# Kernel tuning notes

Hardware: AMD Instinct MI355X
Metric: run time of the kernel (lower is better)

The kernel has to match this reference:

```python
import jax, jax.numpy as jnp
import numpy as np

B, T, C = 16, 1024, 128  # batch, block_size (window length), n_hembd


def setup_inputs() -> dict:
    key = jax.random.key(0)
    k1, k2, k3 = jax.random.split(key, 3)
    Q = jax.random.normal(k1, (B, T, C), dtype=jnp.float32)
    K = jax.random.normal(k2, (B, 2 * T - 1, C), dtype=jnp.float32)
    # learned parameter keyWindowBias: (1, 1, n_hembd, block_size)
    bias = jax.random.normal(k3, (1, 1, C, T), dtype=jnp.float32)
    return {"Q": Q, "K": K, "bias": bias}


def reference(Q, K, bias):
    # Original: K_sw = K.unfold(1, T, 1) -> (B, T, C, T) with K_sw[b,w,c,t] = K[b,w+t,c]
    #           Z = einsum('bwc,bwct->bwt', Q, K_sw + bias)
    # Distribute the dot product over the bias add to avoid materializing (B,T,C,T):
    #   Z[b,w,t] = sum_c Q[b,w,c] * K[b,w+t,c]  +  sum_c Q[b,w,c] * bias[c,t]
    Bn, Tn, Cn = Q.shape
    # Dense scores against all 2T-1 key positions: (B, T, 2T-1)
    S = jnp.einsum('bwc,bkc->bwk', Q, K)
    # Gather sliding-window diagonals: idx[w, t] = w + t
    idx = jnp.arange(Tn)[:, None] + jnp.arange(Tn)[None, :]  # (T, T)
    Zk = jnp.take_along_axis(S, idx[None, :, :], axis=2)      # (B, T, T)
    # Bias contribution: Q @ bias, shared across windows
    Zb = jnp.einsum('bwc,ct->bwt', Q, bias[0, 0])             # (B, T, T)
    return Zk + Zb
```

## Files before the change

### kernel.cpp

```cpp
#include <hip/hip_runtime.h>
#include <hip/hip_bf16.h>


#define B_    16
#define T_    1024
#define C_    128
#define KT_   2047

#define BW    32
#define BT    64
#define KROWS 96
#define SS_LD 98

typedef unsigned short ushort_t;
typedef short bf16x8 __attribute__((ext_vector_type(8)));
typedef float f32x4  __attribute__((ext_vector_type(4)));

__device__ __forceinline__ unsigned short f2bf(float f) {
  unsigned int u = __float_as_uint(f);
  u += 0x7FFFu + ((u >> 16) & 1u);
  return (unsigned short)(u >> 16);
}

typedef const __attribute__((address_space(1))) unsigned int* gas_ptr;
typedef __attribute__((address_space(3))) unsigned int* las_ptr;
__device__ __forceinline__ void async_copy16(const void* g, void* l) {
  __builtin_amdgcn_global_load_lds((gas_ptr)g, (las_ptr)l, 16, 0, 0);
}

__device__ __forceinline__ const bf16x8* frag(const ushort_t* t, int row, int kc) {
  return (const bf16x8*)(t + (((row << 4) + (kc ^ (row & 7))) << 3));
}

#define QN4 524288
#define KN4 1048064
#define BN4 32768

__global__ __launch_bounds__(256) void prepass(
    const float* __restrict__ Q, const float* __restrict__ K,
    const float* __restrict__ bias, ushort_t* __restrict__ Qb,
    ushort_t* __restrict__ Kb, ushort_t* __restrict__ bT) {
  int idx = blockIdx.x * 256 + threadIdx.x;
  if (idx < QN4) {
    float4 v = ((const float4*)Q)[idx];
    ((ushort4*)Qb)[idx] = make_ushort4(f2bf(v.x), f2bf(v.y), f2bf(v.z), f2bf(v.w));
  } else if (idx < QN4 + KN4) {
    int i = idx - QN4;
    float4 v = ((const float4*)K)[i];
    ((ushort4*)Kb)[i] = make_ushort4(f2bf(v.x), f2bf(v.y), f2bf(v.z), f2bf(v.w));
  } else if (idx < QN4 + KN4 + BN4) {
    int i = idx - (QN4 + KN4);
    int c = i >> 8;
    int g = i & 255;
    float4 v = ((const float4*)(bias + c * T_))[g];
    int t = g << 2;
    bT[(t + 0) * C_ + c] = f2bf(v.x);
    bT[(t + 1) * C_ + c] = f2bf(v.y);
    bT[(t + 2) * C_ + c] = f2bf(v.z);
    bT[(t + 3) * C_ + c] = f2bf(v.w);
  }
}

__global__ __launch_bounds__(256) void swmm_main(
    const ushort_t* __restrict__ Qb, const ushort_t* __restrict__ Kb,
    const ushort_t* __restrict__ bT, float* __restrict__ out) {
  __shared__ __align__(16) ushort_t tile[3072 * 8];

  const int b  = blockIdx.z;
  const int w0 = blockIdx.y * BW;
  const int t0 = blockIdx.x * BT;
  const int kbase = w0 + t0;
  const int tid = threadIdx.x;
  const int wv = tid >> 6, lane = tid & 63;

#pragma unroll
  for (int seg = 0; seg < 12; ++seg) {
    int slot = seg * 256 + tid;
    int r = slot >> 4;
    int c = (slot & 15) ^ (r & 7);
    const ushort_t* g;
    if (seg < 2) {
      g = Qb + (((size_t)(b * T_ + w0 + r)) << 7) + (c << 3);
    } else if (seg < 8) {
      int gk = kbase + (r - 32);
      if (gk > KT_ - 1) gk = KT_ - 1;
      g = Kb + ((size_t)b * KT_ + gk) * C_ + (c << 3);
    } else {
      g = bT + (((size_t)(t0 + r - 128)) << 7) + (c << 3);
    }
    async_copy16(g, &tile[(size_t)(seg * 256 + wv * 64) * 8]);
  }
  __syncthreads();

  const int frow = lane & 15;
  const int quad = lane >> 4;
  const int drow4 = quad * 4;

  f32x4 bacc[2];
#pragma unroll
  for (int q = 0; q < 2; ++q) {
    int idx = wv + q * 4;
    int m0 = (idx >> 2) * 16, j0 = (idx & 3) * 16;
    f32x4 acc = {0.f, 0.f, 0.f, 0.f};
#pragma unroll
    for (int kk = 0; kk < 4; ++kk) {
      int kc = kk * 4 + quad;
      bf16x8 a  = *frag(tile, m0 + frow, kc);
      bf16x8 bb = *frag(tile, 128 + j0 + frow, kc);
      acc = __builtin_amdgcn_mfma_f32_16x16x32_bf16(a, bb, acc, 0, 0, 0);
    }
    bacc[q] = acc;
  }
  __syncthreads();

  float* Ss = (float*)&tile[2048 * 8];
#pragma unroll
  for (int q = 0; q < 3; ++q) {
    int s = wv + q * 4;
    int mb = s / 6, nn = s % 6;
    int m0 = mb * 16, n0 = nn * 16;
    f32x4 acc = {0.f, 0.f, 0.f, 0.f};
#pragma unroll
    for (int kk = 0; kk < 4; ++kk) {
      int kc = kk * 4 + quad;
      bf16x8 a  = *frag(tile, m0 + frow, kc);
      bf16x8 bb = *frag(tile, 32 + n0 + frow, kc);
      acc = __builtin_amdgcn_mfma_f32_16x16x32_bf16(a, bb, acc, 0, 0, 0);
    }
#pragma unroll
    for (int r = 0; r < 4; ++r)
      Ss[(m0 + drow4 + r) * SS_LD + n0 + frow] = acc[r];
  }
  __syncthreads();

#pragma unroll
  for (int q = 0; q < 2; ++q) {
    int idx = wv + q * 4;
    int m0 = (idx >> 2) * 16, j0 = (idx & 3) * 16;
#pragma unroll
    for (int r = 0; r < 4; ++r) {
      int i = m0 + drow4 + r;
      int j = j0 + frow;
      out[(size_t)(b * T_ + w0 + i) * T_ + t0 + j] = bacc[q][r] + Ss[i * SS_LD + i + j];
    }
  }
}

#define LDB 136
__global__ __launch_bounds__(256) void swmm_fallback(
    const float* __restrict__ Q, const float* __restrict__ K,
    const float* __restrict__ bias, float* __restrict__ out) {
  __shared__ __align__(16) unsigned short Qs[BW * LDB];
  __shared__ __align__(16) unsigned short Ks[KROWS * LDB];
  __shared__ __align__(16) unsigned short Bs[BT * LDB];
  __shared__ __align__(16) float Ss[BW * SS_LD];

  const int b   = blockIdx.z;
  const int w0  = blockIdx.y * BW;
  const int t0  = blockIdx.x * BT;
  const int kbase = w0 + t0;
  const int tid = threadIdx.x;

  {
    const float4* src = (const float4*)(Q + (size_t)(b * T_ + w0) * C_);
    for (int v = tid; v < BW * (C_ / 4); v += 256) {
      int r = v >> 5, cc = v & 31;
      float4 q = src[r * 32 + cc];
      unsigned short* d = &Qs[r * LDB + (cc << 2)];
      d[0] = f2bf(q.x); d[1] = f2bf(q.y); d[2] = f2bf(q.z); d[3] = f2bf(q.w);
    }
  }
  {
    for (int v = tid; v < KROWS * (C_ / 4); v += 256) {
      int r = v >> 5, cc = v & 31;
      int g = kbase + r;
      float4 kv = make_float4(0.f, 0.f, 0.f, 0.f);
      if (g < KT_) kv = ((const float4*)(K + ((size_t)b * KT_ + g) * C_))[cc];
      unsigned short* d = &Ks[r * LDB + (cc << 2)];
      d[0] = f2bf(kv.x); d[1] = f2bf(kv.y); d[2] = f2bf(kv.z); d[3] = f2bf(kv.w);
    }
  }
  {
    for (int v = tid; v < C_ * (BT / 4); v += 256) {
      int c = v >> 4, jj = v & 15;
      float4 bv = ((const float4*)(bias + (size_t)c * T_ + t0))[jj];
      int j4 = jj << 2;
      Bs[(j4 + 0) * LDB + c] = f2bf(bv.x);
      Bs[(j4 + 1) * LDB + c] = f2bf(bv.y);
      Bs[(j4 + 2) * LDB + c] = f2bf(bv.z);
      Bs[(j4 + 3) * LDB + c] = f2bf(bv.w);
    }
  }
  __syncthreads();

  const int wv    = tid >> 6;
  const int lane  = tid & 63;
  const int frow  = lane & 15;
  const int koff  = (lane >> 4) * 8;
  const int drow4 = (lane >> 4) * 4;
  const int NS = KROWS / 16;

  for (int s = wv; s < 2 * NS; s += 4) {
    int mb = s / NS, nn = s % NS;
    int m0 = mb * 16, n0 = nn * 16;
    const unsigned short* arow = &Qs[(m0 + frow) * LDB + koff];
    const unsigned short* brow = &Ks[(n0 + frow) * LDB + koff];
    f32x4 acc = {0.f, 0.f, 0.f, 0.f};
#pragma unroll
    for (int k0 = 0; k0 < C_; k0 += 32) {
      bf16x8 a  = *(const bf16x8*)(arow + k0);
      bf16x8 bb = *(const bf16x8*)(brow + k0);
      acc = __builtin_amdgcn_mfma_f32_16x16x32_bf16(a, bb, acc, 0, 0, 0);
    }
#pragma unroll
    for (int r = 0; r < 4; ++r)
      Ss[(m0 + drow4 + r) * SS_LD + n0 + frow] = acc[r];
  }

  f32x4 bacc[2];
#pragma unroll
  for (int q = 0; q < 2; ++q) {
    int idx = wv + q * 4;
    int m0 = (idx >> 2) * 16, j0 = (idx & 3) * 16;
    const unsigned short* arow = &Qs[(m0 + frow) * LDB + koff];
    const unsigned short* brow = &Bs[(j0 + frow) * LDB + koff];
    f32x4 acc = {0.f, 0.f, 0.f, 0.f};
#pragma unroll
    for (int k0 = 0; k0 < C_; k0 += 32) {
      bf16x8 a  = *(const bf16x8*)(arow + k0);
      bf16x8 bb = *(const bf16x8*)(brow + k0);
      acc = __builtin_amdgcn_mfma_f32_16x16x32_bf16(a, bb, acc, 0, 0, 0);
    }
    bacc[q] = acc;
  }
  __syncthreads();

#pragma unroll
  for (int q = 0; q < 2; ++q) {
    int idx = wv + q * 4;
    int m0 = (idx >> 2) * 16, j0 = (idx & 3) * 16;
#pragma unroll
    for (int r = 0; r < 4; ++r) {
      int i = m0 + drow4 + r;
      int j = j0 + frow;
      out[(size_t)(b * T_ + w0 + i) * T_ + t0 + j] = bacc[q][r] + Ss[i * SS_LD + i + j];
    }
  }
}

extern "C" void kernel_launch(void* const* d_in, const int* in_sizes, int n_in,
                              void* d_out, int out_size, void* d_ws, size_t ws_size,
                              hipStream_t stream) {
  const float* Q    = (const float*)d_in[0];
  const float* K    = (const float*)d_in[1];
  const float* bias = (const float*)d_in[2];
  float* out = (float*)d_out;

  const size_t QB = (size_t)B_ * T_ * C_ * 2;
  const size_t KB = (size_t)B_ * KT_ * C_ * 2;
  const size_t TB = (size_t)T_ * C_ * 2;
  dim3 grid(T_ / BT, T_ / BW, B_);

  if (ws_size >= QB + KB + TB) {
    ushort_t* Qb = (ushort_t*)d_ws;
    ushort_t* Kb = (ushort_t*)((char*)d_ws + QB);
    ushort_t* bT = (ushort_t*)((char*)d_ws + QB + KB);
    prepass<<<(QN4 + KN4 + BN4) / 256, 256, 0, stream>>>(Q, K, bias, Qb, Kb, bT);
    swmm_main<<<grid, dim3(256), 0, stream>>>(Qb, Kb, bT, out);
  } else {
    swmm_fallback<<<grid, dim3(256), 0, stream>>>(Q, K, bias, out);
  }
}
```

Before: 122.1 us.

## Use 32x32x16 MFMA with 5 waves splitting key and bias work

Restructures the main kernel to run 5 waves per block, each computing one 32x32 tile with the 32x32x16 bf16 MFMA. Three waves compute the Q·K window scores into a separate shared-memory score buffer, and two waves compute the Q·bias tile and write the output. This drops one of the two block barriers, since the score buffer no longer aliases the input tile. The cost is a larger shared-memory footprint and an odd wave count per block, which may reduce occupancy and leaves the two output waves waiting on the score waves.

```diff
diff --git a/kernel.cpp b/kernel.cpp
--- a/kernel.cpp
+++ b/kernel.cpp
@@ -9,12 +9,13 @@
 
 #define BW    32
 #define BT    64
-#define KROWS 96
 #define SS_LD 98
+#define NSLOT 3072
 
 typedef unsigned short ushort_t;
 typedef short bf16x8 __attribute__((ext_vector_type(8)));
 typedef float f32x4  __attribute__((ext_vector_type(4)));
+typedef float f32x16 __attribute__((ext_vector_type(16)));
 
 __device__ __forceinline__ unsigned short f2bf(float f) {
   unsigned int u = __float_as_uint(f);
@@ -61,99 +62,80 @@
   }
 }
 
-__global__ __launch_bounds__(256) void swmm_main(
+__global__ __launch_bounds__(320) void swmm_main(
     const ushort_t* __restrict__ Qb, const ushort_t* __restrict__ Kb,
     const ushort_t* __restrict__ bT, float* __restrict__ out) {
-  __shared__ __align__(16) ushort_t tile[3072 * 8];
+  __shared__ __align__(16) ushort_t tile[NSLOT * 8];
+  __shared__ __align__(16) float Ss[BW * SS_LD];
 
   const int b  = blockIdx.z;
   const int w0 = blockIdx.y * BW;
   const int t0 = blockIdx.x * BT;
   const int kbase = w0 + t0;
-  const int tid = threadIdx.x;
-  const int wv = tid >> 6, lane = tid & 63;
-
-#pragma unroll
-  for (int seg = 0; seg < 12; ++seg) {
-    int slot = seg * 256 + tid;
+  const int tid  = threadIdx.x;
+  const int wv   = tid >> 6;
+  const int lane = tid & 63;
+
+  for (int slot = tid; slot < NSLOT; slot += 320) {
     int r = slot >> 4;
     int c = (slot & 15) ^ (r & 7);
     const ushort_t* g;
-    if (seg < 2) {
+    if (r < 32) {
       g = Qb + (((size_t)(b * T_ + w0 + r)) << 7) + (c << 3);
-    } else if (seg < 8) {
+    } else if (r < 128) {
       int gk = kbase + (r - 32);
       if (gk > KT_ - 1) gk = KT_ - 1;
       g = Kb + ((size_t)b * KT_ + gk) * C_ + (c << 3);
     } else {
       g = bT + (((size_t)(t0 + r - 128)) << 7) + (c << 3);
     }
-    async_copy16(g, &tile[(size_t)(seg * 256 + wv * 64) * 8]);
-  }
-  __syncthreads();
-
-  const int frow = lane & 15;
-  const int quad = lane >> 4;
-  const int drow4 = quad * 4;
-
-  f32x4 bacc[2];
-#pragma unroll
-  for (int q = 0; q < 2; ++q) {
-    int idx = wv + q * 4;
-    int m0 = (idx >> 2) * 16, j0 = (idx & 3) * 16;
-    f32x4 acc = {0.f, 0.f, 0.f, 0.f};
-#pragma unroll
-    for (int kk = 0; kk < 4; ++kk) {
-      int kc = kk * 4 + quad;
-      bf16x8 a  = *frag(tile, m0 + frow, kc);
-      bf16x8 bb = *frag(tile, 128 + j0 + frow, kc);
-      acc = __builtin_amdgcn_mfma_f32_16x16x32_bf16(a, bb, acc, 0, 0, 0);
-    }
-    bacc[q] = acc;
-  }
-  __syncthreads();
-
-  float* Ss = (float*)&tile[2048 * 8];
-#pragma unroll
-  for (int q = 0; q < 3; ++q) {
-    int s = wv + q * 4;
-    int mb = s / 6, nn = s % 6;
-    int m0 = mb * 16, n0 = nn * 16;
-    f32x4 acc = {0.f, 0.f, 0.f, 0.f};
-#pragma unroll
-    for (int kk = 0; kk < 4; ++kk) {
-      int kc = kk * 4 + quad;
-      bf16x8 a  = *frag(tile, m0 + frow, kc);
-      bf16x8 bb = *frag(tile, 32 + n0 + frow, kc);
-      acc = __builtin_amdgcn_mfma_f32_16x16x32_bf16(a, bb, acc, 0, 0, 0);
-    }
-#pragma unroll
-    for (int r = 0; r < 4; ++r)
-      Ss[(m0 + drow4 + r) * SS_LD + n0 + frow] = acc[r];
-  }
-  __syncthreads();
-
-#pragma unroll
-  for (int q = 0; q < 2; ++q) {
-    int idx = wv + q * 4;
-    int m0 = (idx >> 2) * 16, j0 = (idx & 3) * 16;
-#pragma unroll
-    for (int r = 0; r < 4; ++r) {
-      int i = m0 + drow4 + r;
-      int j = j0 + frow;
-      out[(size_t)(b * T_ + w0 + i) * T_ + t0 + j] = bacc[q][r] + Ss[i * SS_LD + i + j];
+    async_copy16(g, &tile[(size_t)(slot - lane) * 8]);
+  }
+  __syncthreads();
+
+  const int half = lane >> 5;
+  const int l31  = lane & 31;
+  const int n0   = wv * 32;
+  const int arow = l31;
+  const int brow = (wv < 3) ? (32 + n0 + l31) : (128 + (n0 - 96) + l31);
+
+  f32x16 acc = {};
+#pragma unroll
+  for (int s = 0; s < 8; ++s) {
+    int kc = 2 * s + half;
+    bf16x8 a  = *frag(tile, arow, kc);
+    bf16x8 bb = *frag(tile, brow, kc);
+    acc = __builtin_amdgcn_mfma_f32_32x32x16_bf16(a, bb, acc, 0, 0, 0);
+  }
+
+  if (wv < 3) {
+#pragma unroll
+    for (int r = 0; r < 16; ++r) {
+      int row = (r & 3) + 8 * (r >> 2) + 4 * half;
+      Ss[row * SS_LD + n0 + l31] = acc[r];
+    }
+  }
+  __syncthreads();
+
+  if (wv >= 3) {
+    int j = (wv - 3) * 32 + l31;
+#pragma unroll
+    for (int r = 0; r < 16; ++r) {
+      int i = (r & 3) + 8 * (r >> 2) + 4 * half;
+      out[(size_t)(b * T_ + w0 + i) * T_ + t0 + j] = acc[r] + Ss[i * SS_LD + i + j];
     }
   }
 }
 
 #define LDB 136
+#define KROWS 96
 __global__ __launch_bounds__(256) void swmm_fallback(
     const float* __restrict__ Q, const float* __restrict__ K,
     const float* __restrict__ bias, float* __restrict__ out) {
   __shared__ __align__(16) unsigned short Qs[BW * LDB];
   __shared__ __align__(16) unsigned short Ks[KROWS * LDB];
   __shared__ __align__(16) unsigned short Bs[BT * LDB];
-  __shared__ __align__(16) float Ss[BW * SS_LD];
+  __shared__ __align__(16) float Ssf[BW * SS_LD];
 
   const int b   = blockIdx.z;
   const int w0  = blockIdx.y * BW;
@@ -202,9 +184,9 @@
 
   for (int s = wv; s < 2 * NS; s += 4) {
     int mb = s / NS, nn = s % NS;
-    int m0 = mb * 16, n0 = nn * 16;
+    int m0 = mb * 16, nn0 = nn * 16;
     const unsigned short* arow = &Qs[(m0 + frow) * LDB + koff];
-    const unsigned short* brow = &Ks[(n0 + frow) * LDB + koff];
+    const unsigned short* brow = &Ks[(nn0 + frow) * LDB + koff];
     f32x4 acc = {0.f, 0.f, 0.f, 0.f};
 #pragma unroll
     for (int k0 = 0; k0 < C_; k0 += 32) {
@@ -214,7 +196,7 @@
     }
 #pragma unroll
     for (int r = 0; r < 4; ++r)
-      Ss[(m0 + drow4 + r) * SS_LD + n0 + frow] = acc[r];
+      Ssf[(m0 + drow4 + r) * SS_LD + nn0 + frow] = acc[r];
   }
 
   f32x4 bacc[2];
@@ -243,7 +225,7 @@
     for (int r = 0; r < 4; ++r) {
       int i = m0 + drow4 + r;
       int j = j0 + frow;
-      out[(size_t)(b * T_ + w0 + i) * T_ + t0 + j] = bacc[q][r] + Ss[i * SS_LD + i + j];
+      out[(size_t)(b * T_ + w0 + i) * T_ + t0 + j] = bacc[q][r] + Ssf[i * SS_LD + i + j];
     }
   }
 }
@@ -266,7 +248,7 @@
     ushort_t* Kb = (ushort_t*)((char*)d_ws + QB);
     ushort_t* bT = (ushort_t*)((char*)d_ws + QB + KB);
     prepass<<<(QN4 + KN4 + BN4) / 256, 256, 0, stream>>>(Q, K, bias, Qb, Kb, bT);
-    swmm_main<<<grid, dim3(256), 0, stream>>>(Qb, Kb, bT, out);
+    swmm_main<<<grid, dim3(320), 0, stream>>>(Qb, Kb, bT, out);
   } else {
     swmm_fallback<<<grid, dim3(256), 0, stream>>>(Q, K, bias, out);
   }
```

New measurement: 148.3 us. 21.5% more time.
